# Performance work log

Measured on AMD Instinct MI355X. Metric: run time of the kernel, lower is better.

The kernel has to match this reference:

```python
import jax, jax.numpy as jnp
import numpy as np
from jax import lax

B, T, D = 512, 1024, 64          # batch, timesteps, input_size
H, L, C = 32, 1, 4               # hidden_layer_size, latent_dim, categorical_dim
IN0 = D + L * C                  # lstm layer-0 input dim


def setup_inputs() -> dict:
    key = jax.random.key(0)
    ks = jax.random.split(key, 12)
    bound = 1.0 / np.sqrt(H)     # torch LSTM/Linear default uniform init
    u = lambda k, sh: jax.random.uniform(k, sh, jnp.float32, -bound, bound)

    states = jax.random.normal(ks[0], (B, T, D), jnp.float32)
    tau = jnp.float32(1.0)
    # pre-sampled standard Gumbel noise, time-major [T, B, L, C]
    un = jax.random.uniform(ks[1], (T, B, L, C), jnp.float32, 1e-6, 1.0 - 1e-6)
    gumbel = -jnp.log(-jnp.log(un))

    return {
        "states": states, "tau": tau, "gumbel": gumbel,
        # LSTM layer 0 (input = D + L*C)
        "w_ih0": u(ks[2], (4 * H, IN0)), "w_hh0": u(ks[3], (4 * H, H)),
        "b_ih0": u(ks[4], (4 * H,)),     "b_hh0": u(ks[5], (4 * H,)),
        # LSTM layer 1
        "w_ih1": u(ks[6], (4 * H, H)),   "w_hh1": u(ks[7], (4 * H, H)),
        "b_ih1": u(ks[8], (4 * H,)),     "b_hh1": u(ks[9], (4 * H,)),
        # output linear; bias initialized to eye(C)[0] per init_params
        "w_lin": u(ks[10], (L * C, H)),
        "b_lin": jnp.eye(C, dtype=jnp.float32)[0],
    }


def _lstm_cell(x, h, c, w_ih, w_hh, b_ih, b_hh):
    z = x @ w_ih.T + h @ w_hh.T + (b_ih + b_hh)   # [B, 4H], torch gate order i,f,g,o
    i, f, g, o = jnp.split(z, 4, axis=-1)
    c2 = jax.nn.sigmoid(f) * c + jax.nn.sigmoid(i) * jnp.tanh(g)
    h2 = jax.nn.sigmoid(o) * jnp.tanh(c2)
    return h2, c2


def reference(states, tau, gumbel, w_ih0, w_hh0, b_ih0, b_hh0,
              w_ih1, w_hh1, b_ih1, b_hh1, w_lin, b_lin):
    Bsz = states.shape[0]
    # init_states: zero hidden/cell, c_t = one-hot(0) tiled -> [B, L*C]
    c0 = jnp.tile(jnp.eye(C, dtype=states.dtype)[0], (Bsz, L))
    zeros = jnp.zeros((Bsz, H), states.dtype)
    carry0 = (zeros, zeros, zeros, zeros, c0)

    def step(carry, inp):
        h1, c1, h2, c2, ct = carry
        x_t, g_t = inp                                  # [B,D], [B,L,C]
        x = jnp.concatenate([x_t, ct], axis=-1)         # [B, D+L*C]
        h1, c1 = _lstm_cell(x, h1, c1, w_ih0, w_hh0, b_ih0, b_hh0)
        h2, c2 = _lstm_cell(h1, h2, c2, w_ih1, w_hh1, b_ih1, b_hh1)
        q = h2 @ w_lin.T + b_lin                        # [B, L*C]
        logits = q.reshape(Bsz, L, C)
        # soft gumbel-softmax (module in training mode -> hard=False)
        y = jax.nn.softmax((logits + g_t) / tau, axis=-1)
        ct = y.reshape(Bsz, L * C)
        return (h1, c1, h2, c2, ct), ct

    xs = (jnp.transpose(states, (1, 0, 2)), gumbel)     # time-major
    _, ys = lax.scan(step, carry0, xs)                  # [T, B, L*C]
    return jnp.transpose(ys, (1, 0, 2))                 # [B, T, L*C]
```

## Files before the change

### kernel.cpp

```cpp
#include <hip/hip_runtime.h>

#define BB 512
#define TT 1024
#define DD 64
#define HH 32
#define CC 4
#define TILE 16
#define NT (TT / TILE)

typedef float f4 __attribute__((ext_vector_type(4)));
typedef _Float16 hv2 __attribute__((ext_vector_type(2)));

#define LOG2E 1.4426950408889634f
#define TWO_LOG2E 2.8853900817779268f

__device__ __forceinline__ float rcpf(float x) { return __builtin_amdgcn_rcpf(x); }
__device__ __forceinline__ float ex2(float x) { return __builtin_amdgcn_exp2f(x); }
__device__ __forceinline__ float sigm2(float x) { return rcpf(1.0f + ex2(-x)); }
__device__ __forceinline__ float tanh2(float x) {
    return 1.0f - 2.0f * rcpf(ex2(x + x) + 1.0f);
}
__device__ __forceinline__ float tanh_c(float c) {
    return 1.0f - 2.0f * rcpf(ex2(c * TWO_LOG2E) + 1.0f);
}
__device__ __forceinline__ float pk2(float a, float b) {
    hv2 t; t.x = (_Float16)a; t.y = (_Float16)b;
    return __builtin_bit_cast(float, t);
}
__device__ __forceinline__ hv2 bch(float x) { return __builtin_bit_cast(hv2, x); }
__device__ __forceinline__ float fdot2(float w, float h, float c) {
    return __builtin_amdgcn_fdot2(bch(w), bch(h), c, false);
}

#define DOT32(a0, a1, a2, a3, W, H4)                    \
    _Pragma("unroll")                                   \
    for (int k2 = 0; k2 < 4; ++k2) {                    \
        f4 h_ = H4[k2];                                 \
        a0 = fdot2(W[4 * k2 + 0], h_.x, a0);            \
        a1 = fdot2(W[4 * k2 + 1], h_.y, a1);            \
        a2 = fdot2(W[4 * k2 + 2], h_.z, a2);            \
        a3 = fdot2(W[4 * k2 + 3], h_.w, a3);            \
    }

#define COMBINE(zA, zB, zi, zf, zg, zo)                 \
    {                                                   \
        float pA_ = __shfl_xor(zA, 32, 64);             \
        float pB_ = __shfl_xor(zB, 32, 64);             \
        zi = half ? pA_ : zA; zf = half ? zA : pA_;     \
        zg = half ? pB_ : zB; zo = half ? zB : pB_;     \
    }

__global__ void __launch_bounds__(128, 4)
zx_gemm(const float* __restrict__ states,
        const float* __restrict__ w_ih0,
        const float* __restrict__ b_ih0,
        const float* __restrict__ b_hh0,
        float* __restrict__ zx)
{
    const int b = blockIdx.y;
    const int tile = blockIdx.x;
    const int tid = threadIdx.x;
    __shared__ __align__(16) float xs[16][DD];

    const int tbase = tile * 16;
#pragma unroll
    for (int i = 0; i < 2; ++i) {
        int f = i * 128 + tid;
        int row = f >> 4, c4 = f & 15;
        int t = tbase + row; if (t > TT - 1) t = TT - 1;
        ((f4*)xs)[f] = *(const f4*)(states + ((size_t)b * TT + t) * DD + c4 * 4);
    }
    __syncthreads();

    const int r = tid;
    const f4* wr = (const f4*)(w_ih0 + (size_t)r * 68);
    f4 w[16];
#pragma unroll
    for (int k = 0; k < 16; ++k) w[k] = wr[k];
    const float bias = b_ih0[r] + b_hh0[r];

    for (int i = 0; i < 16; ++i) {
        int t = tbase + i;
        if (t >= TT) break;
        const f4* xv = (const f4*)xs[i];
        float a0 = bias, a1 = 0.f, a2 = 0.f, a3 = 0.f;
#pragma unroll
        for (int k = 0; k < 16; ++k) {
            f4 x4 = xv[k];
            a0 = fmaf(w[k].x, x4.x, a0);
            a1 = fmaf(w[k].y, x4.y, a1);
            a2 = fmaf(w[k].z, x4.z, a2);
            a3 = fmaf(w[k].w, x4.w, a3);
        }
        zx[((size_t)b * TT + t) * 128 + r] = ((a0 + a1) + (a2 + a3)) * LOG2E;
    }
}

__global__ void __launch_bounds__(64, 1)
lstm_pipe(const float* __restrict__ zx,
          const float* __restrict__ taup,
          const float* __restrict__ gumbel,
          const float* __restrict__ w_ih0,
          const float* __restrict__ w_hh0,
          const float* __restrict__ w_ih1,
          const float* __restrict__ w_hh1,
          const float* __restrict__ b_ih1,
          const float* __restrict__ b_hh1,
          const float* __restrict__ w_lin,
          const float* __restrict__ b_lin,
          float* __restrict__ out)
{
    const int b    = blockIdx.x;
    const int l    = threadIdx.x;
    const int half = l >> 5;
    const int rA   = l;
    const int rB   = l + 64;
    const int c    = l >> 4;

    __shared__ __align__(16) float zbuf[2][TILE][128];
    __shared__ __align__(16) float4 gbuf[2][TILE];
    __shared__ __align__(16) _Float16 h1h[HH];
    __shared__ __align__(16) _Float16 h2h[HH];

    const float inv_tau = rcpf(taup[0]);
    const float gs = LOG2E * inv_tau;

    f4 wctA = *(const f4*)(w_ih0 + (size_t)rA * 68 + 64);
    f4 wctB = *(const f4*)(w_ih0 + (size_t)rB * 68 + 64);
    wctA *= LOG2E; wctB *= LOG2E;
    float wh0A[16], wh0B[16], wi1A[16], wi1B[16], wh1A[16], wh1B[16], wlc[16];
#pragma unroll
    for (int k = 0; k < 8; ++k) {
        f4 w;
        w = *(const f4*)(w_hh0 + (size_t)rA * HH + 4 * k) * LOG2E;
        wh0A[2 * k] = pk2(w.x, w.y); wh0A[2 * k + 1] = pk2(w.z, w.w);
        w = *(const f4*)(w_hh0 + (size_t)rB * HH + 4 * k) * LOG2E;
        wh0B[2 * k] = pk2(w.x, w.y); wh0B[2 * k + 1] = pk2(w.z, w.w);
        w = *(const f4*)(w_ih1 + (size_t)rA * HH + 4 * k) * LOG2E;
        wi1A[2 * k] = pk2(w.x, w.y); wi1A[2 * k + 1] = pk2(w.z, w.w);
        w = *(const f4*)(w_ih1 + (size_t)rB * HH + 4 * k) * LOG2E;
        wi1B[2 * k] = pk2(w.x, w.y); wi1B[2 * k + 1] = pk2(w.z, w.w);
        w = *(const f4*)(w_hh1 + (size_t)rA * HH + 4 * k) * LOG2E;
        wh1A[2 * k] = pk2(w.x, w.y); wh1A[2 * k + 1] = pk2(w.z, w.w);
        w = *(const f4*)(w_hh1 + (size_t)rB * HH + 4 * k) * LOG2E;
        wh1B[2 * k] = pk2(w.x, w.y); wh1B[2 * k + 1] = pk2(w.z, w.w);
        w = *(const f4*)(w_lin + (size_t)c * HH + 4 * k) * gs;
        wlc[2 * k] = pk2(w.x, w.y); wlc[2 * k + 1] = pk2(w.z, w.w);
    }
    const float bias1A = (b_ih1[rA] + b_hh1[rA]) * LOG2E;
    const float bias1B = (b_ih1[rB] + b_hh1[rB]) * LOG2E;
    const float blc = b_lin[c] * gs;

    const float* __restrict__ zb = zx + (size_t)b * TT * 128;
    float* __restrict__ ob = out + (size_t)b * TT * CC;
    const int srow = l >> 5;
    const int scol = l & 31;

    {
        f4 sz[8];
#pragma unroll
        for (int i = 0; i < 8; ++i) {
            int row = 1 + i * 2 + srow;
            sz[i] = *(const f4*)(zb + (size_t)row * 128 + scol * 4);
        }
        float4 gv = *(const float4*)(gumbel + ((size_t)(l & 15) * BB + b) * CC);
        gv.x *= gs; gv.y *= gs; gv.z *= gs; gv.w *= gs;
#pragma unroll
        for (int i = 0; i < 8; ++i) ((f4*)&zbuf[0][0][0])[i * 64 + l] = sz[i];
        if (l < 16) gbuf[0][l] = gv;
    }

    float cst1 = 0.f, cst2 = 0.f;
    f4 h1g[4];

    {
        float zA = zb[rA] + wctA.x;
        float zB = zb[rB] + wctB.x;
        float zi, zf, zg, zo;
        COMBINE(zA, zB, zi, zf, zg, zo);
        (void)zf;
        cst1 = sigm2(zi) * tanh2(zg);
        float h1n = sigm2(zo) * tanh_c(cst1);
        if (l < HH) h1h[l] = (_Float16)h1n;
#pragma unroll
        for (int k2 = 0; k2 < 4; ++k2) h1g[k2] = ((const f4*)h1h)[k2];

        float bA0 = bias1A, bA1 = 0.f, bA2 = 0.f, bA3 = 0.f;
        float bB0 = bias1B, bB1 = 0.f, bB2 = 0.f, bB3 = 0.f;
        DOT32(bA0, bA1, bA2, bA3, wi1A, h1g);
        DOT32(bB0, bB1, bB2, bB3, wi1B, h1g);
        zA = (bA0 + bA1) + (bA2 + bA3);
        zB = (bB0 + bB1) + (bB2 + bB3);
        COMBINE(zA, zB, zi, zf, zg, zo);
        cst2 = sigm2(zi) * tanh2(zg);
        float h2n = sigm2(zo) * tanh_c(cst2);
        if (l < HH) h2h[l] = (_Float16)h2n;
    }

    for (int k = 0; k < NT; ++k) {
        const int cb = k & 1, nb = cb ^ 1;
        const int kn = (k + 1 < NT) ? k + 1 : 0;
        float4 gv;

#pragma unroll
        for (int hf = 0; hf < 2; ++hf) {
            f4 szh[4];
#pragma unroll
            for (int i = 0; i < 4; ++i) {
                int ii = hf * 4 + i;
                int row = kn * TILE + 1 + ii * 2 + srow;
                if (row > TT - 1) row = TT - 1;
                szh[i] = *(const f4*)(zb + (size_t)row * 128 + scol * 4);
            }
            if (hf == 0)
                gv = *(const float4*)(gumbel +
                        ((size_t)(kn * TILE + (l & 15)) * BB + b) * CC);

#pragma unroll 2
            for (int s8 = 0; s8 < 8; ++s8) {
                const int s = hf * 8 + s8;
                const int t = k * TILE + s;

                const float zxnA = zbuf[cb][s][rA];
                const float zxnB = zbuf[cb][s][rB];
                const float4 gtc = gbuf[cb][s];
                f4 h2g[4];
#pragma unroll
                for (int k2 = 0; k2 < 4; ++k2) h2g[k2] = ((const f4*)h2h)[k2];

                float aA0 = 0.f, aA1 = 0.f, aA2 = 0.f, aA3 = 0.f;
                float aB0 = 0.f, aB1 = 0.f, aB2 = 0.f, aB3 = 0.f;
                DOT32(aA0, aA1, aA2, aA3, wh0A, h1g);
                DOT32(aB0, aB1, aB2, aB3, wh0B, h1g);

                float s0 = blc, s1 = 0.f, s2 = 0.f, s3 = 0.f;
                DOT32(s0, s1, s2, s3, wlc, h2g);
                float qown = (s0 + s1) + (s2 + s3);

                float t1 = __shfl_xor(qown, 16, 64);
                float t2 = __shfl_xor(qown, 32, 64);
                float t3 = __shfl_xor(qown, 48, 64);
                float q0 = (c == 0) ? qown : (c == 1) ? t1 : (c == 2) ? t2 : t3;
                float q1 = (c == 0) ? t1 : (c == 1) ? qown : (c == 2) ? t3 : t2;
                float q2 = (c == 0) ? t2 : (c == 1) ? t3 : (c == 2) ? qown : t1;
                float q3 = (c == 0) ? t3 : (c == 1) ? t2 : (c == 2) ? t1 : qown;
                float e0 = ex2(q0 + gtc.x);
                float e1 = ex2(q1 + gtc.y);
                float e2 = ex2(q2 + gtc.z);
                float e3 = ex2(q3 + gtc.w);
                float inv = rcpf((e0 + e1) + (e2 + e3));
                if (l == 0)
                    *(float4*)(ob + (size_t)t * CC) =
                        make_float4(e0 * inv, e1 * inv, e2 * inv, e3 * inv);

                float weA0 = wctA.x * e0, weA1 = wctA.y * e1;
                float weA2 = wctA.z * e2, weA3 = wctA.w * e3;
                float weB0 = wctB.x * e0, weB1 = wctB.y * e1;
                float weB2 = wctB.z * e2, weB3 = wctB.w * e3;
                aA0 = fmaf(weA0, inv, aA0 + zxnA); aA1 = fmaf(weA1, inv, aA1);
                aA2 = fmaf(weA2, inv, aA2);        aA3 = fmaf(weA3, inv, aA3);
                aB0 = fmaf(weB0, inv, aB0 + zxnB); aB1 = fmaf(weB1, inv, aB1);
                aB2 = fmaf(weB2, inv, aB2);        aB3 = fmaf(weB3, inv, aB3);
                float zA = (aA0 + aA1) + (aA2 + aA3);
                float zB = (aB0 + aB1) + (aB2 + aB3);
                float zi, zf, zg, zo;
                COMBINE(zA, zB, zi, zf, zg, zo);
                cst1 = fmaf(sigm2(zf), cst1, sigm2(zi) * tanh2(zg));
                float h1n = sigm2(zo) * tanh_c(cst1);
                if (l < HH) h1h[l] = (_Float16)h1n;

#pragma unroll
                for (int k2 = 0; k2 < 4; ++k2) h1g[k2] = ((const f4*)h1h)[k2];

                float bA0 = bias1A, bA1 = 0.f, bA2 = 0.f, bA3 = 0.f;
                float bB0 = bias1B, bB1 = 0.f, bB2 = 0.f, bB3 = 0.f;
                DOT32(bA0, bA1, bA2, bA3, wh1A, h2g);
                DOT32(bB0, bB1, bB2, bB3, wh1B, h2g);
                DOT32(bA0, bA1, bA2, bA3, wi1A, h1g);
                DOT32(bB0, bB1, bB2, bB3, wi1B, h1g);
                zA = (bA0 + bA1) + (bA2 + bA3);
                zB = (bB0 + bB1) + (bB2 + bB3);
                COMBINE(zA, zB, zi, zf, zg, zo);
                cst2 = fmaf(sigm2(zf), cst2, sigm2(zi) * tanh2(zg));
                float h2n = sigm2(zo) * tanh_c(cst2);
                if (l < HH) h2h[l] = (_Float16)h2n;
            }

#pragma unroll
            for (int i = 0; i < 4; ++i)
                ((f4*)&zbuf[nb][0][0])[(hf * 4 + i) * 64 + l] = szh[i];
        }
        gv.x *= gs; gv.y *= gs; gv.z *= gs; gv.w *= gs;
        if (l < 16) gbuf[nb][l] = gv;

        asm volatile("" : "+v"(wh0A[0]), "+v"(wh0A[1]), "+v"(wh0A[2]), "+v"(wh0A[3]),
                          "+v"(wh0A[4]), "+v"(wh0A[5]), "+v"(wh0A[6]), "+v"(wh0A[7]),
                          "+v"(wh0A[8]), "+v"(wh0A[9]), "+v"(wh0A[10]), "+v"(wh0A[11]),
                          "+v"(wh0A[12]), "+v"(wh0A[13]), "+v"(wh0A[14]), "+v"(wh0A[15]));
        asm volatile("" : "+v"(wh0B[0]), "+v"(wh0B[1]), "+v"(wh0B[2]), "+v"(wh0B[3]),
                          "+v"(wh0B[4]), "+v"(wh0B[5]), "+v"(wh0B[6]), "+v"(wh0B[7]),
                          "+v"(wh0B[8]), "+v"(wh0B[9]), "+v"(wh0B[10]), "+v"(wh0B[11]),
                          "+v"(wh0B[12]), "+v"(wh0B[13]), "+v"(wh0B[14]), "+v"(wh0B[15]));
        asm volatile("" : "+v"(wi1A[0]), "+v"(wi1A[1]), "+v"(wi1A[2]), "+v"(wi1A[3]),
                          "+v"(wi1A[4]), "+v"(wi1A[5]), "+v"(wi1A[6]), "+v"(wi1A[7]),
                          "+v"(wi1A[8]), "+v"(wi1A[9]), "+v"(wi1A[10]), "+v"(wi1A[11]),
                          "+v"(wi1A[12]), "+v"(wi1A[13]), "+v"(wi1A[14]), "+v"(wi1A[15]));
        asm volatile("" : "+v"(wi1B[0]), "+v"(wi1B[1]), "+v"(wi1B[2]), "+v"(wi1B[3]),
                          "+v"(wi1B[4]), "+v"(wi1B[5]), "+v"(wi1B[6]), "+v"(wi1B[7]),
                          "+v"(wi1B[8]), "+v"(wi1B[9]), "+v"(wi1B[10]), "+v"(wi1B[11]),
                          "+v"(wi1B[12]), "+v"(wi1B[13]), "+v"(wi1B[14]), "+v"(wi1B[15]));
        asm volatile("" : "+v"(wh1A[0]), "+v"(wh1A[1]), "+v"(wh1A[2]), "+v"(wh1A[3]),
                          "+v"(wh1A[4]), "+v"(wh1A[5]), "+v"(wh1A[6]), "+v"(wh1A[7]),
                          "+v"(wh1A[8]), "+v"(wh1A[9]), "+v"(wh1A[10]), "+v"(wh1A[11]),
                          "+v"(wh1A[12]), "+v"(wh1A[13]), "+v"(wh1A[14]), "+v"(wh1A[15]));
        asm volatile("" : "+v"(wh1B[0]), "+v"(wh1B[1]), "+v"(wh1B[2]), "+v"(wh1B[3]),
                          "+v"(wh1B[4]), "+v"(wh1B[5]), "+v"(wh1B[6]), "+v"(wh1B[7]),
                          "+v"(wh1B[8]), "+v"(wh1B[9]), "+v"(wh1B[10]), "+v"(wh1B[11]),
                          "+v"(wh1B[12]), "+v"(wh1B[13]), "+v"(wh1B[14]), "+v"(wh1B[15]));
        asm volatile("" : "+v"(wlc[0]), "+v"(wlc[1]), "+v"(wlc[2]), "+v"(wlc[3]),
                          "+v"(wlc[4]), "+v"(wlc[5]), "+v"(wlc[6]), "+v"(wlc[7]),
                          "+v"(wlc[8]), "+v"(wlc[9]), "+v"(wlc[10]), "+v"(wlc[11]),
                          "+v"(wlc[12]), "+v"(wlc[13]), "+v"(wlc[14]), "+v"(wlc[15]));
        asm volatile("" : "+v"(wctA), "+v"(wctB));
    }
}

extern "C" __global__ void __launch_bounds__(128, 2)
lstm_opt_enc(const float* __restrict__ states, const float* __restrict__ taup,
             const float* __restrict__ gumbel, const float* __restrict__ w_ih0,
             const float* __restrict__ w_hh0, const float* __restrict__ b_ih0,
             const float* __restrict__ b_hh0, const float* __restrict__ w_ih1,
             const float* __restrict__ w_hh1, const float* __restrict__ b_ih1,
             const float* __restrict__ b_hh1, const float* __restrict__ w_lin,
             const float* __restrict__ b_lin, float* __restrict__ out)
{
    const int b   = blockIdx.x;
    const int tid = threadIdx.x;
    const int l   = tid & 63;
    const int wv  = tid >> 6;
    const int u0  = l & 15;
    const int g   = l >> 4;
    const int u   = wv * 16 + u0;
    const int r   = g * 32 + u;

    __shared__ __align__(16) float xb[2][DD];
    __shared__ __align__(16) float h1b[2][HH];
    __shared__ __align__(16) float h2b[2][HH];

    float wi0r[68], wh0r[HH], wi1r[HH], wh1r[HH];
#pragma unroll
    for (int k = 0; k < 68; ++k) wi0r[k] = w_ih0[r * 68 + k];
#pragma unroll
    for (int k = 0; k < HH; ++k) wh0r[k] = w_hh0[r * HH + k];
#pragma unroll
    for (int k = 0; k < HH; ++k) wi1r[k] = w_ih1[r * HH + k];
#pragma unroll
    for (int k = 0; k < HH; ++k) wh1r[k] = w_hh1[r * HH + k];
    const float bias0 = b_ih0[r] + b_hh0[r];
    const float bias1 = b_ih1[r] + b_hh1[r];
    const float inv_tau = __builtin_amdgcn_rcpf(taup[0]);
    const float wl0 = w_lin[g * HH + u0];
    const float wl1 = w_lin[g * HH + u0 + 16];
    const float blc = b_lin[g];

    float cst1 = 0.f, cst2 = 0.f;
    float y0 = 1.f, y1 = 0.f, y2 = 0.f, y3 = 0.f;

    const float* __restrict__ sb = states + (size_t)b * TT * DD;
    float* __restrict__ ob = out + (size_t)b * TT * CC;

    float xr = 0.f;
    if (tid < DD) xr = sb[tid];
    if (tid < HH) { h1b[0][tid] = 0.f; h2b[0][tid] = 0.f; }
    if (tid < DD) { xb[0][tid] = xr; xr = sb[DD + tid]; }
    __syncthreads();

    for (int t = 0; t < TT; ++t) {
        const int p = t & 1, np = p ^ 1;
        if (tid < DD) { xb[np][tid] = xr; }
        const int tn = (t + 2 < TT) ? t + 2 : TT - 1;
        if (tid < DD) { xr = sb[tn * DD + tid]; }
        const float4 gt = *(const float4*)(gumbel + ((size_t)t * BB + b) * CC);

        float a0 = bias0, a1 = 0.f, a2 = 0.f, a3 = 0.f;
        const float4* xv = (const float4*)xb[p];
#pragma unroll
        for (int k = 0; k < 16; ++k) {
            float4 x4 = xv[k];
            a0 = fmaf(wi0r[4 * k + 0], x4.x, a0);
            a1 = fmaf(wi0r[4 * k + 1], x4.y, a1);
            a2 = fmaf(wi0r[4 * k + 2], x4.z, a2);
            a3 = fmaf(wi0r[4 * k + 3], x4.w, a3);
        }
        a0 = fmaf(wi0r[64], y0, a0);
        a1 = fmaf(wi0r[65], y1, a1);
        a2 = fmaf(wi0r[66], y2, a2);
        a3 = fmaf(wi0r[67], y3, a3);
        const float4* h1v = (const float4*)h1b[p];
#pragma unroll
        for (int k = 0; k < 8; ++k) {
            float4 h4 = h1v[k];
            a0 = fmaf(wh0r[4 * k + 0], h4.x, a0);
            a1 = fmaf(wh0r[4 * k + 1], h4.y, a1);
            a2 = fmaf(wh0r[4 * k + 2], h4.z, a2);
            a3 = fmaf(wh0r[4 * k + 3], h4.w, a3);
        }
        float z = (a0 + a1) + (a2 + a3);
        float v1  = __shfl_xor(z, 16, 64);
        float lo  = (g & 1) ? v1 : z;
        float hi  = (g & 1) ? z  : v1;
        float lo2 = __shfl_xor(lo, 32, 64);
        float hi2 = __shfl_xor(hi, 32, 64);
        float zi = (g < 2) ? lo  : lo2;
        float zf = (g < 2) ? hi  : hi2;
        float zg = (g < 2) ? lo2 : lo;
        float zo = (g < 2) ? hi2 : hi;
        float sf = __builtin_amdgcn_rcpf(1.0f + __expf(-zf));
        float si = __builtin_amdgcn_rcpf(1.0f + __expf(-zi));
        float tg = 1.0f - 2.0f * __builtin_amdgcn_rcpf(__expf(2.0f * zg) + 1.0f);
        float so = __builtin_amdgcn_rcpf(1.0f + __expf(-zo));
        cst1 = sf * cst1 + si * tg;
        float h1new = so * (1.0f - 2.0f * __builtin_amdgcn_rcpf(__expf(2.0f * cst1) + 1.0f));
        if (g == 0) h1b[np][u] = h1new;
        __syncthreads();

        a0 = bias1; a1 = 0.f; a2 = 0.f; a3 = 0.f;
        const float4* h1n = (const float4*)h1b[np];
        const float4* h2v = (const float4*)h2b[p];
#pragma unroll
        for (int k = 0; k < 8; ++k) {
            float4 h4 = h1n[k];
            float4 g4 = h2v[k];
            a0 = fmaf(wi1r[4 * k + 0], h4.x, a0);
            a1 = fmaf(wi1r[4 * k + 1], h4.y, a1);
            a2 = fmaf(wi1r[4 * k + 2], h4.z, a2);
            a3 = fmaf(wi1r[4 * k + 3], h4.w, a3);
            a0 = fmaf(wh1r[4 * k + 0], g4.x, a0);
            a1 = fmaf(wh1r[4 * k + 1], g4.y, a1);
            a2 = fmaf(wh1r[4 * k + 2], g4.z, a2);
            a3 = fmaf(wh1r[4 * k + 3], g4.w, a3);
        }
        z = (a0 + a1) + (a2 + a3);
        v1  = __shfl_xor(z, 16, 64);
        lo  = (g & 1) ? v1 : z;
        hi  = (g & 1) ? z  : v1;
        lo2 = __shfl_xor(lo, 32, 64);
        hi2 = __shfl_xor(hi, 32, 64);
        zi = (g < 2) ? lo  : lo2;
        zf = (g < 2) ? hi  : hi2;
        zg = (g < 2) ? lo2 : lo;
        zo = (g < 2) ? hi2 : hi;
        sf = __builtin_amdgcn_rcpf(1.0f + __expf(-zf));
        si = __builtin_amdgcn_rcpf(1.0f + __expf(-zi));
        tg = 1.0f - 2.0f * __builtin_amdgcn_rcpf(__expf(2.0f * zg) + 1.0f);
        so = __builtin_amdgcn_rcpf(1.0f + __expf(-zo));
        cst2 = sf * cst2 + si * tg;
        float h2new = so * (1.0f - 2.0f * __builtin_amdgcn_rcpf(__expf(2.0f * cst2) + 1.0f));
        if (g == 0) h2b[np][u] = h2new;
        __syncthreads();

        float part = wl0 * h2b[np][u0] + wl1 * h2b[np][u0 + 16];
        part += __shfl_xor(part, 1, 64);
        part += __shfl_xor(part, 2, 64);
        part += __shfl_xor(part, 4, 64);
        part += __shfl_xor(part, 8, 64);
        float qown = part + blc;
        float t1 = __shfl_xor(qown, 16, 64);
        float t2 = __shfl_xor(qown, 32, 64);
        float t3 = __shfl_xor(t1, 32, 64);
        float q0 = (g == 0) ? qown : (g == 1) ? t1 : (g == 2) ? t2 : t3;
        float q1 = (g == 0) ? t1 : (g == 1) ? qown : (g == 2) ? t3 : t2;
        float q2 = (g == 0) ? t2 : (g == 1) ? t3 : (g == 2) ? qown : t1;
        float q3 = (g == 0) ? t3 : (g == 1) ? t2 : (g == 2) ? t1 : qown;
        float l0  = (q0 + gt.x) * inv_tau;
        float l1_ = (q1 + gt.y) * inv_tau;
        float l2  = (q2 + gt.z) * inv_tau;
        float l3  = (q3 + gt.w) * inv_tau;
        float m = fmaxf(fmaxf(l0, l1_), fmaxf(l2, l3));
        float e0 = __expf(l0 - m), e1 = __expf(l1_ - m);
        float e2 = __expf(l2 - m), e3 = __expf(l3 - m);
        float inv = __builtin_amdgcn_rcpf((e0 + e1) + (e2 + e3));
        y0 = e0 * inv; y1 = e1 * inv; y2 = e2 * inv; y3 = e3 * inv;

        if (tid == 0) *(float4*)(ob + (size_t)t * CC) = make_float4(y0, y1, y2, y3);
    }
}

extern "C" void kernel_launch(void* const* d_in, const int* in_sizes, int n_in,
                              void* d_out, int out_size, void* d_ws, size_t ws_size,
                              hipStream_t stream) {
    const float* states = (const float*)d_in[0];
    const float* tau    = (const float*)d_in[1];
    const float* gumbel = (const float*)d_in[2];
    const float* w_ih0  = (const float*)d_in[3];
    const float* w_hh0  = (const float*)d_in[4];
    const float* b_ih0  = (const float*)d_in[5];
    const float* b_hh0  = (const float*)d_in[6];
    const float* w_ih1  = (const float*)d_in[7];
    const float* w_hh1  = (const float*)d_in[8];
    const float* b_ih1  = (const float*)d_in[9];
    const float* b_hh1  = (const float*)d_in[10];
    const float* w_lin  = (const float*)d_in[11];
    const float* b_lin  = (const float*)d_in[12];
    float* out = (float*)d_out;

    const size_t zx_bytes = (size_t)BB * TT * 128 * 4;
    if (ws_size >= zx_bytes) {
        float* zx = (float*)d_ws;
        hipLaunchKernelGGL(zx_gemm, dim3(TT / 16, BB), dim3(128), 0, stream,
                           states, w_ih0, b_ih0, b_hh0, zx);
        hipLaunchKernelGGL(lstm_pipe, dim3(BB), dim3(64), 0, stream,
                           zx, tau, gumbel, w_ih0, w_hh0, w_ih1, w_hh1,
                           b_ih1, b_hh1, w_lin, b_lin, out);
    } else {
        hipLaunchKernelGGL(lstm_opt_enc, dim3(BB), dim3(128), 0, stream,
                           states, tau, gumbel, w_ih0, w_hh0, b_ih0, b_hh0,
                           w_ih1, w_hh1, b_ih1, b_hh1, w_lin, b_lin, out);
    }
}
```

Before: 926.4 us.

## Interleave two batch sequences per wavefront in the LSTM recurrence kernel

The recurrent kernel now processes two batch rows per 64-lane block, with duplicated LDS buffers, state and dot products, and launches half as many blocks. The aim is to hide the latency of the serial per-timestep dependency chain with instruction-level parallelism from two independent recurrences. It raises register and LDS use per wave and reduces the number of resident waves, and the hardware may already have been overlapping separate waves on the same CU. The inner loop unroll also drops from 2 to 1.

Result: slower. 1.485 ms (+60.3%).

```diff
diff --git a/kernel.cpp b/kernel.cpp
--- a/kernel.cpp
+++ b/kernel.cpp
@@ -49,6 +49,10 @@
         zi = half ? pA_ : zA; zf = half ? zA : pA_;     \
         zg = half ? pB_ : zB; zo = half ? zB : pB_;     \
     }
+
+#define GATHER4(dst, srcLDS)                            \
+    _Pragma("unroll")                                   \
+    for (int k2 = 0; k2 < 4; ++k2) dst[k2] = ((const f4*)(srcLDS))[k2];
 
 __global__ void __launch_bounds__(128, 4)
 zx_gemm(const float* __restrict__ states,
@@ -97,30 +101,31 @@
 }
 
 __global__ void __launch_bounds__(64, 1)
-lstm_pipe(const float* __restrict__ zx,
-          const float* __restrict__ taup,
-          const float* __restrict__ gumbel,
-          const float* __restrict__ w_ih0,
-          const float* __restrict__ w_hh0,
-          const float* __restrict__ w_ih1,
-          const float* __restrict__ w_hh1,
-          const float* __restrict__ b_ih1,
-          const float* __restrict__ b_hh1,
-          const float* __restrict__ w_lin,
-          const float* __restrict__ b_lin,
-          float* __restrict__ out)
+lstm_pipe2(const float* __restrict__ zx,
+           const float* __restrict__ taup,
+           const float* __restrict__ gumbel,
+           const float* __restrict__ w_ih0,
+           const float* __restrict__ w_hh0,
+           const float* __restrict__ w_ih1,
+           const float* __restrict__ w_hh1,
+           const float* __restrict__ b_ih1,
+           const float* __restrict__ b_hh1,
+           const float* __restrict__ w_lin,
+           const float* __restrict__ b_lin,
+           float* __restrict__ out)
 {
-    const int b    = blockIdx.x;
+    const int b0   = 2 * (int)blockIdx.x;
+    const int b1   = b0 + 1;
     const int l    = threadIdx.x;
     const int half = l >> 5;
     const int rA   = l;
     const int rB   = l + 64;
     const int c    = l >> 4;
 
-    __shared__ __align__(16) float zbuf[2][TILE][128];
-    __shared__ __align__(16) float4 gbuf[2][TILE];
-    __shared__ __align__(16) _Float16 h1h[HH];
-    __shared__ __align__(16) _Float16 h2h[HH];
+    __shared__ __align__(16) float zbufs[2][2][TILE][128];
+    __shared__ __align__(16) float4 gbufs[2][2][TILE];
+    __shared__ __align__(16) _Float16 h1hs[2][HH];
+    __shared__ __align__(16) _Float16 h2hs[2][HH];
 
     const float inv_tau = rcpf(taup[0]);
     const float gs = LOG2E * inv_tau;
@@ -151,147 +156,239 @@
     const float bias1B = (b_ih1[rB] + b_hh1[rB]) * LOG2E;
     const float blc = b_lin[c] * gs;
 
-    const float* __restrict__ zb = zx + (size_t)b * TT * 128;
-    float* __restrict__ ob = out + (size_t)b * TT * CC;
+    const float* __restrict__ zb0 = zx + (size_t)b0 * TT * 128;
+    const float* __restrict__ zb1 = zx + (size_t)b1 * TT * 128;
+    float* __restrict__ ob0 = out + (size_t)b0 * TT * CC;
+    float* __restrict__ ob1 = out + (size_t)b1 * TT * CC;
     const int srow = l >> 5;
     const int scol = l & 31;
 
     {
-        f4 sz[8];
+        f4 sz0[8], sz1[8];
 #pragma unroll
         for (int i = 0; i < 8; ++i) {
             int row = 1 + i * 2 + srow;
-            sz[i] = *(const f4*)(zb + (size_t)row * 128 + scol * 4);
+            sz0[i] = *(const f4*)(zb0 + (size_t)row * 128 + scol * 4);
+            sz1[i] = *(const f4*)(zb1 + (size_t)row * 128 + scol * 4);
         }
-        float4 gv = *(const float4*)(gumbel + ((size_t)(l & 15) * BB + b) * CC);
-        gv.x *= gs; gv.y *= gs; gv.z *= gs; gv.w *= gs;
-#pragma unroll
-        for (int i = 0; i < 8; ++i) ((f4*)&zbuf[0][0][0])[i * 64 + l] = sz[i];
-        if (l < 16) gbuf[0][l] = gv;
-    }
-
-    float cst1 = 0.f, cst2 = 0.f;
-    f4 h1g[4];
+        float4 gv0 = *(const float4*)(gumbel + ((size_t)(l & 15) * BB + b0) * CC);
+        float4 gv1 = *(const float4*)(gumbel + ((size_t)(l & 15) * BB + b1) * CC);
+        gv0.x *= gs; gv0.y *= gs; gv0.z *= gs; gv0.w *= gs;
+        gv1.x *= gs; gv1.y *= gs; gv1.z *= gs; gv1.w *= gs;
+#pragma unroll
+        for (int i = 0; i < 8; ++i) {
+            ((f4*)&zbufs[0][0][0][0])[i * 64 + l] = sz0[i];
+            ((f4*)&zbufs[1][0][0][0])[i * 64 + l] = sz1[i];
+        }
+        if (l < 16) { gbufs[0][0][l] = gv0; gbufs[1][0][l] = gv1; }
+    }
+
+    float cs10 = 0.f, cs20 = 0.f, cs11 = 0.f, cs21 = 0.f;
+    f4 h1g0[4], h1g1[4];
 
     {
-        float zA = zb[rA] + wctA.x;
-        float zB = zb[rB] + wctB.x;
+        float zA = zb0[rA] + wctA.x;
+        float zB = zb0[rB] + wctB.x;
         float zi, zf, zg, zo;
         COMBINE(zA, zB, zi, zf, zg, zo);
         (void)zf;
-        cst1 = sigm2(zi) * tanh2(zg);
-        float h1n = sigm2(zo) * tanh_c(cst1);
-        if (l < HH) h1h[l] = (_Float16)h1n;
-#pragma unroll
-        for (int k2 = 0; k2 < 4; ++k2) h1g[k2] = ((const f4*)h1h)[k2];
-
+        cs10 = sigm2(zi) * tanh2(zg);
+        float h1n = sigm2(zo) * tanh_c(cs10);
+        if (l < HH) h1hs[0][l] = (_Float16)h1n;
+        GATHER4(h1g0, h1hs[0]);
         float bA0 = bias1A, bA1 = 0.f, bA2 = 0.f, bA3 = 0.f;
         float bB0 = bias1B, bB1 = 0.f, bB2 = 0.f, bB3 = 0.f;
-        DOT32(bA0, bA1, bA2, bA3, wi1A, h1g);
-        DOT32(bB0, bB1, bB2, bB3, wi1B, h1g);
+        DOT32(bA0, bA1, bA2, bA3, wi1A, h1g0);
+        DOT32(bB0, bB1, bB2, bB3, wi1B, h1g0);
         zA = (bA0 + bA1) + (bA2 + bA3);
         zB = (bB0 + bB1) + (bB2 + bB3);
         COMBINE(zA, zB, zi, zf, zg, zo);
-        cst2 = sigm2(zi) * tanh2(zg);
-        float h2n = sigm2(zo) * tanh_c(cst2);
-        if (l < HH) h2h[l] = (_Float16)h2n;
+        cs20 = sigm2(zi) * tanh2(zg);
+        float h2n = sigm2(zo) * tanh_c(cs20);
+        if (l < HH) h2hs[0][l] = (_Float16)h2n;
+    }
+    {
+        float zA = zb1[rA] + wctA.x;
+        float zB = zb1[rB] + wctB.x;
+        float zi, zf, zg, zo;
+        COMBINE(zA, zB, zi, zf, zg, zo);
+        (void)zf;
+        cs11 = sigm2(zi) * tanh2(zg);
+        float h1n = sigm2(zo) * tanh_c(cs11);
+        if (l < HH) h1hs[1][l] = (_Float16)h1n;
+        GATHER4(h1g1, h1hs[1]);
+        float bA0 = bias1A, bA1 = 0.f, bA2 = 0.f, bA3 = 0.f;
+        float bB0 = bias1B, bB1 = 0.f, bB2 = 0.f, bB3 = 0.f;
+        DOT32(bA0, bA1, bA2, bA3, wi1A, h1g1);
+        DOT32(bB0, bB1, bB2, bB3, wi1B, h1g1);
+        zA = (bA0 + bA1) + (bA2 + bA3);
+        zB = (bB0 + bB1) + (bB2 + bB3);
+        COMBINE(zA, zB, zi, zf, zg, zo);
+        cs21 = sigm2(zi) * tanh2(zg);
+        float h2n = sigm2(zo) * tanh_c(cs21);
+        if (l < HH) h2hs[1][l] = (_Float16)h2n;
     }
 
     for (int k = 0; k < NT; ++k) {
         const int cb = k & 1, nb = cb ^ 1;
         const int kn = (k + 1 < NT) ? k + 1 : 0;
-        float4 gv;
+        float4 gv0, gv1;
 
 #pragma unroll
         for (int hf = 0; hf < 2; ++hf) {
-            f4 szh[4];
+            f4 szh0[4], szh1[4];
 #pragma unroll
             for (int i = 0; i < 4; ++i) {
                 int ii = hf * 4 + i;
                 int row = kn * TILE + 1 + ii * 2 + srow;
                 if (row > TT - 1) row = TT - 1;
-                szh[i] = *(const f4*)(zb + (size_t)row * 128 + scol * 4);
+                szh0[i] = *(const f4*)(zb0 + (size_t)row * 128 + scol * 4);
+                szh1[i] = *(const f4*)(zb1 + (size_t)row * 128 + scol * 4);
             }
-            if (hf == 0)
-                gv = *(const float4*)(gumbel +
-                        ((size_t)(kn * TILE + (l & 15)) * BB + b) * CC);
-
-#pragma unroll 2
+            if (hf == 0) {
+                gv0 = *(const float4*)(gumbel +
+                        ((size_t)(kn * TILE + (l & 15)) * BB + b0) * CC);
+                gv1 = *(const float4*)(gumbel +
+                        ((size_t)(kn * TILE + (l & 15)) * BB + b1) * CC);
+            }
+
+#pragma unroll 1
             for (int s8 = 0; s8 < 8; ++s8) {
                 const int s = hf * 8 + s8;
                 const int t = k * TILE + s;
 
-                const float zxnA = zbuf[cb][s][rA];
-                const float zxnB = zbuf[cb][s][rB];
-                const float4 gtc = gbuf[cb][s];
-                f4 h2g[4];
-#pragma unroll
-                for (int k2 = 0; k2 < 4; ++k2) h2g[k2] = ((const f4*)h2h)[k2];
-
-                float aA0 = 0.f, aA1 = 0.f, aA2 = 0.f, aA3 = 0.f;
-                float aB0 = 0.f, aB1 = 0.f, aB2 = 0.f, aB3 = 0.f;
-                DOT32(aA0, aA1, aA2, aA3, wh0A, h1g);
-                DOT32(aB0, aB1, aB2, aB3, wh0B, h1g);
-
-                float s0 = blc, s1 = 0.f, s2 = 0.f, s3 = 0.f;
-                DOT32(s0, s1, s2, s3, wlc, h2g);
-                float qown = (s0 + s1) + (s2 + s3);
-
-                float t1 = __shfl_xor(qown, 16, 64);
-                float t2 = __shfl_xor(qown, 32, 64);
-                float t3 = __shfl_xor(qown, 48, 64);
-                float q0 = (c == 0) ? qown : (c == 1) ? t1 : (c == 2) ? t2 : t3;
-                float q1 = (c == 0) ? t1 : (c == 1) ? qown : (c == 2) ? t3 : t2;
-                float q2 = (c == 0) ? t2 : (c == 1) ? t3 : (c == 2) ? qown : t1;
-                float q3 = (c == 0) ? t3 : (c == 1) ? t2 : (c == 2) ? t1 : qown;
-                float e0 = ex2(q0 + gtc.x);
-                float e1 = ex2(q1 + gtc.y);
-                float e2 = ex2(q2 + gtc.z);
-                float e3 = ex2(q3 + gtc.w);
-                float inv = rcpf((e0 + e1) + (e2 + e3));
-                if (l == 0)
-                    *(float4*)(ob + (size_t)t * CC) =
-                        make_float4(e0 * inv, e1 * inv, e2 * inv, e3 * inv);
-
-                float weA0 = wctA.x * e0, weA1 = wctA.y * e1;
-                float weA2 = wctA.z * e2, weA3 = wctA.w * e3;
-                float weB0 = wctB.x * e0, weB1 = wctB.y * e1;
-                float weB2 = wctB.z * e2, weB3 = wctB.w * e3;
-                aA0 = fmaf(weA0, inv, aA0 + zxnA); aA1 = fmaf(weA1, inv, aA1);
-                aA2 = fmaf(weA2, inv, aA2);        aA3 = fmaf(weA3, inv, aA3);
-                aB0 = fmaf(weB0, inv, aB0 + zxnB); aB1 = fmaf(weB1, inv, aB1);
-                aB2 = fmaf(weB2, inv, aB2);        aB3 = fmaf(weB3, inv, aB3);
-                float zA = (aA0 + aA1) + (aA2 + aA3);
-                float zB = (aB0 + aB1) + (aB2 + aB3);
-                float zi, zf, zg, zo;
-                COMBINE(zA, zB, zi, zf, zg, zo);
-                cst1 = fmaf(sigm2(zf), cst1, sigm2(zi) * tanh2(zg));
-                float h1n = sigm2(zo) * tanh_c(cst1);
-                if (l < HH) h1h[l] = (_Float16)h1n;
-
-#pragma unroll
-                for (int k2 = 0; k2 < 4; ++k2) h1g[k2] = ((const f4*)h1h)[k2];
-
-                float bA0 = bias1A, bA1 = 0.f, bA2 = 0.f, bA3 = 0.f;
-                float bB0 = bias1B, bB1 = 0.f, bB2 = 0.f, bB3 = 0.f;
-                DOT32(bA0, bA1, bA2, bA3, wh1A, h2g);
-                DOT32(bB0, bB1, bB2, bB3, wh1B, h2g);
-                DOT32(bA0, bA1, bA2, bA3, wi1A, h1g);
-                DOT32(bB0, bB1, bB2, bB3, wi1B, h1g);
-                zA = (bA0 + bA1) + (bA2 + bA3);
-                zB = (bB0 + bB1) + (bB2 + bB3);
-                COMBINE(zA, zB, zi, zf, zg, zo);
-                cst2 = fmaf(sigm2(zf), cst2, sigm2(zi) * tanh2(zg));
-                float h2n = sigm2(zo) * tanh_c(cst2);
-                if (l < HH) h2h[l] = (_Float16)h2n;
+                const float zxnA0 = zbufs[0][cb][s][rA];
+                const float zxnB0 = zbufs[0][cb][s][rB];
+                const float zxnA1 = zbufs[1][cb][s][rA];
+                const float zxnB1 = zbufs[1][cb][s][rB];
+                const float4 gtc0 = gbufs[0][cb][s];
+                const float4 gtc1 = gbufs[1][cb][s];
+                f4 h2g0[4], h2g1[4];
+                GATHER4(h2g0, h2hs[0]);
+                GATHER4(h2g1, h2hs[1]);
+
+                float aA00 = 0.f, aA10 = 0.f, aA20 = 0.f, aA30 = 0.f;
+                float aB00 = 0.f, aB10 = 0.f, aB20 = 0.f, aB30 = 0.f;
+                float aA01 = 0.f, aA11 = 0.f, aA21 = 0.f, aA31 = 0.f;
+                float aB01 = 0.f, aB11 = 0.f, aB21 = 0.f, aB31 = 0.f;
+                DOT32(aA00, aA10, aA20, aA30, wh0A, h1g0);
+                DOT32(aA01, aA11, aA21, aA31, wh0A, h1g1);
+                DOT32(aB00, aB10, aB20, aB30, wh0B, h1g0);
+                DOT32(aB01, aB11, aB21, aB31, wh0B, h1g1);
+
+                float s00 = blc, s10 = 0.f, s20 = 0.f, s30 = 0.f;
+                float s01 = blc, s11 = 0.f, s21 = 0.f, s31 = 0.f;
+                DOT32(s00, s10, s20, s30, wlc, h2g0);
+                DOT32(s01, s11, s21, s31, wlc, h2g1);
+                float qown0 = (s00 + s10) + (s20 + s30);
+                float qown1 = (s01 + s11) + (s21 + s31);
+
+                float t1_0 = __shfl_xor(qown0, 16, 64);
+                float t1_1 = __shfl_xor(qown1, 16, 64);
+                float t2_0 = __shfl_xor(qown0, 32, 64);
+                float t2_1 = __shfl_xor(qown1, 32, 64);
+                float t3_0 = __shfl_xor(t1_0, 32, 64);
+                float t3_1 = __shfl_xor(t1_1, 32, 64);
+                float q00 = (c == 0) ? qown0 : (c == 1) ? t1_0 : (c == 2) ? t2_0 : t3_0;
+                float q10 = (c == 0) ? t1_0 : (c == 1) ? qown0 : (c == 2) ? t3_0 : t2_0;
+                float q20 = (c == 0) ? t2_0 : (c == 1) ? t3_0 : (c == 2) ? qown0 : t1_0;
+                float q30 = (c == 0) ? t3_0 : (c == 1) ? t2_0 : (c == 2) ? t1_0 : qown0;
+                float q01 = (c == 0) ? qown1 : (c == 1) ? t1_1 : (c == 2) ? t2_1 : t3_1;
+                float q11 = (c == 0) ? t1_1 : (c == 1) ? qown1 : (c == 2) ? t3_1 : t2_1;
+                float q21 = (c == 0) ? t2_1 : (c == 1) ? t3_1 : (c == 2) ? qown1 : t1_1;
+                float q31 = (c == 0) ? t3_1 : (c == 1) ? t2_1 : (c == 2) ? t1_1 : qown1;
+                float e00 = ex2(q00 + gtc0.x), e10 = ex2(q10 + gtc0.y);
+                float e20 = ex2(q20 + gtc0.z), e30 = ex2(q30 + gtc0.w);
+                float e01 = ex2(q01 + gtc1.x), e11 = ex2(q11 + gtc1.y);
+                float e21 = ex2(q21 + gtc1.z), e31 = ex2(q31 + gtc1.w);
+                float inv0 = rcpf((e00 + e10) + (e20 + e30));
+                float inv1 = rcpf((e01 + e11) + (e21 + e31));
+                if (l == 0) {
+                    *(float4*)(ob0 + (size_t)t * CC) =
+                        make_float4(e00 * inv0, e10 * inv0, e20 * inv0, e30 * inv0);
+                    *(float4*)(ob1 + (size_t)t * CC) =
+                        make_float4(e01 * inv1, e11 * inv1, e21 * inv1, e31 * inv1);
+                }
+
+                {
+                    float weA0 = wctA.x * e00, weA1 = wctA.y * e10;
+                    float weA2 = wctA.z * e20, weA3 = wctA.w * e30;
+                    float weB0 = wctB.x * e00, weB1 = wctB.y * e10;
+                    float weB2 = wctB.z * e20, weB3 = wctB.w * e30;
+                    aA00 = fmaf(weA0, inv0, aA00 + zxnA0); aA10 = fmaf(weA1, inv0, aA10);
+                    aA20 = fmaf(weA2, inv0, aA20);         aA30 = fmaf(weA3, inv0, aA30);
+                    aB00 = fmaf(weB0, inv0, aB00 + zxnB0); aB10 = fmaf(weB1, inv0, aB10);
+                    aB20 = fmaf(weB2, inv0, aB20);         aB30 = fmaf(weB3, inv0, aB30);
+                    float zA = (aA00 + aA10) + (aA20 + aA30);
+                    float zB = (aB00 + aB10) + (aB20 + aB30);
+                    float zi, zf, zg, zo;
+                    COMBINE(zA, zB, zi, zf, zg, zo);
+                    cs10 = fmaf(sigm2(zf), cs10, sigm2(zi) * tanh2(zg));
+                    float h1n = sigm2(zo) * tanh_c(cs10);
+                    if (l < HH) h1hs[0][l] = (_Float16)h1n;
+                }
+                {
+                    float weA0 = wctA.x * e01, weA1 = wctA.y * e11;
+                    float weA2 = wctA.z * e21, weA3 = wctA.w * e31;
+                    float weB0 = wctB.x * e01, weB1 = wctB.y * e11;
+                    float weB2 = wctB.z * e21, weB3 = wctB.w * e31;
+                    aA01 = fmaf(weA0, inv1, aA01 + zxnA1); aA11 = fmaf(weA1, inv1, aA11);
+                    aA21 = fmaf(weA2, inv1, aA21);         aA31 = fmaf(weA3, inv1, aA31);
+                    aB01 = fmaf(weB0, inv1, aB01 + zxnB1); aB11 = fmaf(weB1, inv1, aB11);
+                    aB21 = fmaf(weB2, inv1, aB21);         aB31 = fmaf(weB3, inv1, aB31);
+                    float zA = (aA01 + aA11) + (aA21 + aA31);
+                    float zB = (aB01 + aB11) + (aB21 + aB31);
+                    float zi, zf, zg, zo;
+                    COMBINE(zA, zB, zi, zf, zg, zo);
+                    cs11 = fmaf(sigm2(zf), cs11, sigm2(zi) * tanh2(zg));
+                    float h1n = sigm2(zo) * tanh_c(cs11);
+                    if (l < HH) h1hs[1][l] = (_Float16)h1n;
+                }
+
+                GATHER4(h1g0, h1hs[0]);
+                GATHER4(h1g1, h1hs[1]);
+
+                {
+                    float bA0 = bias1A, bA1 = 0.f, bA2 = 0.f, bA3 = 0.f;
+                    float bB0 = bias1B, bB1 = 0.f, bB2 = 0.f, bB3 = 0.f;
+                    DOT32(bA0, bA1, bA2, bA3, wh1A, h2g0);
+                    DOT32(bB0, bB1, bB2, bB3, wh1B, h2g0);
+                    DOT32(bA0, bA1, bA2, bA3, wi1A, h1g0);
+                    DOT32(bB0, bB1, bB2, bB3, wi1B, h1g0);
+                    float zA = (bA0 + bA1) + (bA2 + bA3);
+                    float zB = (bB0 + bB1) + (bB2 + bB3);
+                    float zi, zf, zg, zo;
+                    COMBINE(zA, zB, zi, zf, zg, zo);
+                    cs20 = fmaf(sigm2(zf), cs20, sigm2(zi) * tanh2(zg));
+                    float h2n = sigm2(zo) * tanh_c(cs20);
+                    if (l < HH) h2hs[0][l] = (_Float16)h2n;
+                }
+                {
+                    float bA0 = bias1A, bA1 = 0.f, bA2 = 0.f, bA3 = 0.f;
+                    float bB0 = bias1B, bB1 = 0.f, bB2 = 0.f, bB3 = 0.f;
+                    DOT32(bA0, bA1, bA2, bA3, wh1A, h2g1);
+                    DOT32(bB0, bB1, bB2, bB3, wh1B, h2g1);
+                    DOT32(bA0, bA1, bA2, bA3, wi1A, h1g1);
+                    DOT32(bB0, bB1, bB2, bB3, wi1B, h1g1);
+                    float zA = (bA0 + bA1) + (bA2 + bA3);
+                    float zB = (bB0 + bB1) + (bB2 + bB3);
+                    float zi, zf, zg, zo;
+                    COMBINE(zA, zB, zi, zf, zg, zo);
+                    cs21 = fmaf(sigm2(zf), cs21, sigm2(zi) * tanh2(zg));
+                    float h2n = sigm2(zo) * tanh_c(cs21);
+                    if (l < HH) h2hs[1][l] = (_Float16)h2n;
+                }
             }
 
 #pragma unroll
-            for (int i = 0; i < 4; ++i)
-                ((f4*)&zbuf[nb][0][0])[(hf * 4 + i) * 64 + l] = szh[i];
+            for (int i = 0; i < 4; ++i) {
+                ((f4*)&zbufs[0][nb][0][0])[(hf * 4 + i) * 64 + l] = szh0[i];
+                ((f4*)&zbufs[1][nb][0][0])[(hf * 4 + i) * 64 + l] = szh1[i];
+            }
         }
-        gv.x *= gs; gv.y *= gs; gv.z *= gs; gv.w *= gs;
-        if (l < 16) gbuf[nb][l] = gv;
+        gv0.x *= gs; gv0.y *= gs; gv0.z *= gs; gv0.w *= gs;
+        gv1.x *= gs; gv1.y *= gs; gv1.z *= gs; gv1.w *= gs;
+        if (l < 16) { gbufs[0][nb][l] = gv0; gbufs[1][nb][l] = gv1; }
 
         asm volatile("" : "+v"(wh0A[0]), "+v"(wh0A[1]), "+v"(wh0A[2]), "+v"(wh0A[3]),
                           "+v"(wh0A[4]), "+v"(wh0A[5]), "+v"(wh0A[6]), "+v"(wh0A[7]),
@@ -337,9 +434,9 @@
     const int b   = blockIdx.x;
     const int tid = threadIdx.x;
     const int l   = tid & 63;
-    const int wv  = tid >> 6;
     const int u0  = l & 15;
     const int g   = l >> 4;
+    const int wv  = tid >> 6;
     const int u   = wv * 16 + u0;
     const int r   = g * 32 + u;
 
@@ -358,7 +455,7 @@
     for (int k = 0; k < HH; ++k) wh1r[k] = w_hh1[r * HH + k];
     const float bias0 = b_ih0[r] + b_hh0[r];
     const float bias1 = b_ih1[r] + b_hh1[r];
-    const float inv_tau = __builtin_amdgcn_rcpf(taup[0]);
+    const float inv_tau = rcpf(taup[0]);
     const float wl0 = w_lin[g * HH + u0];
     const float wl1 = w_lin[g * HH + u0 + 16];
     const float blc = b_lin[g];
@@ -415,12 +512,12 @@
         float zf = (g < 2) ? hi  : hi2;
         float zg = (g < 2) ? lo2 : lo;
         float zo = (g < 2) ? hi2 : hi;
-        float sf = __builtin_amdgcn_rcpf(1.0f + __expf(-zf));
-        float si = __builtin_amdgcn_rcpf(1.0f + __expf(-zi));
-        float tg = 1.0f - 2.0f * __builtin_amdgcn_rcpf(__expf(2.0f * zg) + 1.0f);
-        float so = __builtin_amdgcn_rcpf(1.0f + __expf(-zo));
+        float sf = rcpf(1.0f + __expf(-zf));
+        float si = rcpf(1.0f + __expf(-zi));
+        float tg = 1.0f - 2.0f * rcpf(__expf(2.0f * zg) + 1.0f);
+        float so = rcpf(1.0f + __expf(-zo));
         cst1 = sf * cst1 + si * tg;
-        float h1new = so * (1.0f - 2.0f * __builtin_amdgcn_rcpf(__expf(2.0f * cst1) + 1.0f));
+        float h1new = so * (1.0f - 2.0f * rcpf(__expf(2.0f * cst1) + 1.0f));
         if (g == 0) h1b[np][u] = h1new;
         __syncthreads();
 
@@ -450,12 +547,12 @@
         zf = (g < 2) ? hi  : hi2;
         zg = (g < 2) ? lo2 : lo;
         zo = (g < 2) ? hi2 : hi;
-        sf = __builtin_amdgcn_rcpf(1.0f + __expf(-zf));
-        si = __builtin_amdgcn_rcpf(1.0f + __expf(-zi));
-        tg = 1.0f - 2.0f * __builtin_amdgcn_rcpf(__expf(2.0f * zg) + 1.0f);
-        so = __builtin_amdgcn_rcpf(1.0f + __expf(-zo));
+        sf = rcpf(1.0f + __expf(-zf));
+        si = rcpf(1.0f + __expf(-zi));
+        tg = 1.0f - 2.0f * rcpf(__expf(2.0f * zg) + 1.0f);
+        so = rcpf(1.0f + __expf(-zo));
         cst2 = sf * cst2 + si * tg;
-        float h2new = so * (1.0f - 2.0f * __builtin_amdgcn_rcpf(__expf(2.0f * cst2) + 1.0f));
+        float h2new = so * (1.0f - 2.0f * rcpf(__expf(2.0f * cst2) + 1.0f));
         if (g == 0) h2b[np][u] = h2new;
         __syncthreads();
 
@@ -479,7 +576,7 @@
         float m = fmaxf(fmaxf(l0, l1_), fmaxf(l2, l3));
         float e0 = __expf(l0 - m), e1 = __expf(l1_ - m);
         float e2 = __expf(l2 - m), e3 = __expf(l3 - m);
-        float inv = __builtin_amdgcn_rcpf((e0 + e1) + (e2 + e3));
+        float inv = rcpf((e0 + e1) + (e2 + e3));
         y0 = e0 * inv; y1 = e1 * inv; y2 = e2 * inv; y3 = e3 * inv;
 
         if (tid == 0) *(float4*)(ob + (size_t)t * CC) = make_float4(y0, y1, y2, y3);
@@ -509,7 +606,7 @@
         float* zx = (float*)d_ws;
         hipLaunchKernelGGL(zx_gemm, dim3(TT / 16, BB), dim3(128), 0, stream,
                            states, w_ih0, b_ih0, b_hh0, zx);
-        hipLaunchKernelGGL(lstm_pipe, dim3(BB), dim3(64), 0, stream,
+        hipLaunchKernelGGL(lstm_pipe2, dim3(BB / 2), dim3(64), 0, stream,
                            zx, tau, gumbel, w_ih0, w_hh0, w_ih1, w_hh1,
                            b_ih1, b_hh1, w_lin, b_lin, out);
     } else {
```
